# Optimization experiments

Hardware: AMD Instinct MI355X
Metric: run time of the kernel (lower is better)

## Reference

```python
import jax, jax.numpy as jnp
import numpy as np

HEADS = 16
EMBED_DIM = 1024
HEAD_DIM = EMBED_DIM // HEADS
N, Q_LEN, KV_LEN = 4, 2048, 2048


def setup_inputs() -> dict:
    key = jax.random.key(0)
    k1, k2, k3, k4, k5, k6 = jax.random.split(key, 6)
    query = jax.random.normal(k1, (N, Q_LEN, EMBED_DIM), dtype=jnp.float32)
    key_t = jax.random.normal(k2, (N, KV_LEN, EMBED_DIM), dtype=jnp.float32)
    value = jax.random.normal(k3, (N, KV_LEN, EMBED_DIM), dtype=jnp.float32)
    mask = jax.random.randint(k4, (N, 1, Q_LEN, KV_LEN), 0, 2, dtype=jnp.int32)
    # output projection (the only Linear actually used in the original forward)
    W_out = jax.random.normal(k5, (EMBED_DIM, EMBED_DIM), dtype=jnp.float32) / np.sqrt(EMBED_DIM)
    b_out = jax.random.normal(k6, (EMBED_DIM,), dtype=jnp.float32) * 0.01
    return {"query": query, "key": key_t, "value": value, "mask": mask,
            "W_out": W_out, "b_out": b_out}


def reference(query, key, value, mask, W_out, b_out):
    n, q_len, _ = query.shape
    k_len = key.shape[1]
    # split heads: [N, L, E] -> [N, L, H, D]
    q = query.reshape(n, q_len, HEADS, HEAD_DIM)
    k = key.reshape(n, k_len, HEADS, HEAD_DIM)
    v = value.reshape(n, k_len, HEADS, HEAD_DIM)
    # full QK^T scores: [N, H, Q, K]
    scores = jnp.einsum("nqhd,nkhd->nhqk", q, k)
    scores = jnp.where(mask == 0, jnp.float32(-1e9), scores)
    # non-canonical scale: 1/sqrt(embed_dim), applied AFTER masking (as original)
    attn = jax.nn.softmax(scores / jnp.sqrt(jnp.float32(EMBED_DIM)), axis=3)
    out = jnp.einsum("nhql,nlhd->nqhd", attn, v).reshape(n, q_len, HEADS * HEAD_DIM)
    return out @ W_out.T + b_out
```

## Files before the change

kernel.cpp:

```cpp
#include <hip/hip_runtime.h>
#include <stdint.h>

#define NB 4
#define QL 2048
#define KL 2048
#define HEADS 16
#define EMB 1024
#define HD 64

typedef float f32x2 __attribute__((ext_vector_type(2)));
typedef float f32x4 __attribute__((ext_vector_type(4)));
typedef float f32x16 __attribute__((ext_vector_type(16)));
typedef __bf16 bf16x2 __attribute__((ext_vector_type(2)));
typedef __bf16 bf16x8 __attribute__((ext_vector_type(8)));
typedef unsigned short u16x8 __attribute__((ext_vector_type(8)));
typedef unsigned short u16x4 __attribute__((ext_vector_type(4)));
typedef unsigned int u32x4 __attribute__((ext_vector_type(4)));

static __device__ __forceinline__ unsigned short f2bf(float f) {
  unsigned u = __float_as_uint(f);
  u += 0x7fffu + ((u >> 16) & 1u);
  return (unsigned short)(u >> 16);
}
static __device__ __forceinline__ float bf2f(unsigned short h) {
  return __uint_as_float(((unsigned)h) << 16);
}
static __device__ __forceinline__ float fast_exp2(float x) {
#if __has_builtin(__builtin_amdgcn_exp2f)
  return __builtin_amdgcn_exp2f(x);
#else
  return __expf(x * 0.6931471805599453f);
#endif
}
static __device__ __forceinline__ float fast_rcp(float x) {
#if __has_builtin(__builtin_amdgcn_rcpf)
  return __builtin_amdgcn_rcpf(x);
#else
  return 1.0f / x;
#endif
}
static __device__ __forceinline__ void dma16(const void* g, void* l) {
  __builtin_amdgcn_global_load_lds(
      (const __attribute__((address_space(1))) unsigned int*)(uintptr_t)g,
      (__attribute__((address_space(3))) unsigned int*)(uintptr_t)l, 16, 0, 0);
}
static __device__ __forceinline__ void dma4(const void* g, void* l) {
  __builtin_amdgcn_global_load_lds(
      (const __attribute__((address_space(1))) unsigned int*)(uintptr_t)g,
      (__attribute__((address_space(3))) unsigned int*)(uintptr_t)l, 4, 0, 0);
}
static __device__ __forceinline__ void barrier_plain() {
  __asm__ volatile("" ::: "memory");
  __builtin_amdgcn_s_barrier();
  __asm__ volatile("" ::: "memory");
}
#define WAITVM(N) __asm__ volatile("s_waitcnt vmcnt(" #N ")" ::: "memory")

#define XHI_OFF  0ull
#define XLO_OFF  16777216ull
#define KHI_OFF  33554432ull
#define VT_OFF   50331648ull
#define WHI_OFF  67108864ull
#define WLO_OFF  69206016ull
#define MB_OFF   71303168ull

#define QSC  0.0450842399f
#define ESHIFT 11.5415601730f

__global__ __launch_bounds__(256) void prep_all(const float* __restrict__ Kg,
                                                const float* __restrict__ Vg,
                                                const float* __restrict__ Wg,
                                                const int* __restrict__ Mg,
                                                unsigned short* __restrict__ Khi,
                                                unsigned short* __restrict__ Vt,
                                                unsigned short* __restrict__ Whi,
                                                unsigned short* __restrict__ Wlo,
                                                unsigned long long* __restrict__ bits) {
  __shared__ unsigned short lds[64 * 66];
  const int tid = threadIdx.x;
  const int bid = blockIdx.x;
  if (bid < 8192) {
    int t = bid * 256 + tid;
    int d4 = t & 15, h = (t >> 4) & 15, kv = (t >> 8) & 2047, n = t >> 19;
    f32x4 a = *(const f32x4*)(Kg + (size_t)(n * KL + kv) * EMB + h * 64 + d4 * 4);
    u16x4 o;
    #pragma unroll
    for (int j = 0; j < 4; ++j) o[j] = f2bf(a[j]);
    int row = kv & 63, c0 = d4 >> 1;
    int pos = row * 128 + ((c0 ^ (row & 7)) << 4) + (d4 & 1) * 8;
    size_t slab = (size_t)((n * 16 + h) * 32 + (kv >> 6)) * 8192;
    *(u16x4*)((char*)Khi + slab + pos) = o;
  } else if (bid < 10240) {
    int vb = bid - 8192;
    int kt = vb & 31, h = (vb >> 5) & 15, n = vb >> 9;
    #pragma unroll
    for (int i = 0; i < 4; ++i) {
      int e = i * 256 + tid;
      int d4 = e & 15, kvl = e >> 4;
      int col = (kvl & 48) | (kvl & 3) | ((kvl & 4) << 1) | ((kvl & 8) >> 1);
      f32x4 a = *(const f32x4*)(Vg + (size_t)(n * KL + kt * 64 + kvl) * EMB + h * 64 + d4 * 4);
      #pragma unroll
      for (int j = 0; j < 4; ++j) lds[(d4 * 4 + j) * 66 + col] = f2bf(a[j]);
    }
    __syncthreads();
    size_t slab = (size_t)((n * 16 + h) * 32 + kt) * 8192;
    #pragma unroll
    for (int i = 0; i < 4; ++i) {
      int e = i * 256 + tid;
      int kv4 = e & 15, d = e >> 4;
      u16x4 o;
      #pragma unroll
      for (int j = 0; j < 4; ++j) o[j] = lds[d * 66 + kv4 * 4 + j];
      int c0 = kv4 >> 1;
      int pos = d * 128 + ((c0 ^ (d & 7)) << 4) + (kv4 & 1) * 8;
      *(u16x4*)((char*)Vt + slab + pos) = o;
    }
  } else if (bid < 11264) {
    int t = (bid - 10240) * 256 + tid;
    int c4 = t & 255, row = t >> 8;
    f32x4 a = *(const f32x4*)(Wg + (size_t)row * 1024 + c4 * 4);
    u16x4 hi, lo;
    #pragma unroll
    for (int j = 0; j < 4; ++j) {
      unsigned short hb = f2bf(a[j]);
      hi[j] = hb;
      lo[j] = f2bf(a[j] - bf2f(hb));
    }
    *(u16x4*)(Whi + (size_t)row * 1024 + c4 * 4) = hi;
    *(u16x4*)(Wlo + (size_t)row * 1024 + c4 * 4) = lo;
  } else {
    int t = (bid - 11264) * 256 + tid;
    int l = t & 63;
    int W = t >> 6;
    int kw2 = (W & 15) * 2;
    int row = W >> 4;
    const int* mp = Mg + (size_t)row * KL;
    int v0 = mp[kw2 * 64 + l];
    int v1 = mp[kw2 * 64 + 64 + l];
    unsigned long long b0 = __ballot(v0 != 0);
    unsigned long long b1 = __ballot(v1 != 0);
    int q = row & 2047, nn = row >> 11;
    size_t base = (size_t)((nn * 8 + (q >> 8)) * 32) * 256 + (q & 255);
    if (l == 0) {
      bits[base + (size_t)kw2 * 256] = b0;
      bits[base + (size_t)(kw2 + 1) * 256] = b1;
    }
  }
}

__global__ __launch_bounds__(256, 2) void attn4(const float* __restrict__ Qg,
                                                const unsigned short* __restrict__ Khi,
                                                const unsigned short* __restrict__ Vt,
                                                const unsigned long long* __restrict__ Mb,
                                                unsigned short* __restrict__ Xhi,
                                                unsigned short* __restrict__ Xlo) {
  __shared__ __align__(16) char smem[2 * 18432];
  const int tid = threadIdx.x;
  const int w = tid >> 6;
  const int l = tid & 63;
  const int q32 = l & 31;
  const int h5 = l >> 5;
  const int bid = blockIdx.x;
  const int qb = bid & 7;
  const int h = (bid >> 3) & 15;
  const int n = bid >> 7;
  const int qbase = qb * 256 + w * 64;

  const char* kslab = (const char*)Khi + (size_t)(n * HEADS + h) * 262144;
  const char* vslab = (const char*)Vt + (size_t)(n * HEADS + h) * 262144;
  const char* mslab = (const char*)Mb + (size_t)(n * 8 + qb) * 65536;

  bf16x8 qh[2][4];
  #pragma unroll
  for (int c = 0; c < 2; ++c) {
    const float* qp = Qg + (size_t)(n * QL + qbase + c * 32 + q32) * EMB + h * HD + h5 * 8;
    #pragma unroll
    for (int kc = 0; kc < 4; ++kc) {
      union { u16x8 u; bf16x8 b; } H;
      #pragma unroll
      for (int j = 0; j < 8; ++j) H.u[j] = f2bf(qp[kc * 16 + j] * QSC);
      qh[c][kc] = H.b;
    }
  }
  WAITVM(0);

  int off8[2][4];
  #pragma unroll
  for (int r2 = 0; r2 < 2; ++r2)
    #pragma unroll
    for (int g = 0; g < 4; ++g)
      off8[r2][g] = (r2 * 32 + q32) * 128 + (((2 * g + h5) ^ (q32 & 7)) << 4);

  f32x16 o00, o01, o10, o11, l0, l1;
  #pragma unroll
  for (int i = 0; i < 16; ++i) {
    o00[i] = 0.f; o01[i] = 0.f; o10[i] = 0.f; o11[i] = 0.f; l0[i] = 0.f; l1[i] = 0.f;
  }

  union { u16x8 u; bf16x8 b; } O1;
  #pragma unroll
  for (int j = 0; j < 8; ++j) O1.u[j] = 0x3F80;
  const bf16x8 ones = O1.b;

  auto issue = [&](int kt, char* buf) {
    const char* ks = kslab + kt * 8192 + w * 2048 + l * 16;
    const char* vs = vslab + kt * 8192 + w * 2048 + l * 16;
    dma16(ks, buf + w * 2048);
    dma16(ks + 1024, buf + w * 2048 + 1024);
    dma16(vs, buf + 8192 + w * 2048);
    dma16(vs + 1024, buf + 8192 + w * 2048 + 1024);
    const char* ms = mslab + kt * 2048 + w * 512 + l * 4;
    dma4(ms, buf + 16384 + w * 512);
    dma4(ms + 256, buf + 16384 + w * 512 + 256);
  };

  auto step = [&](int kt, char* cur, char* nxt) {
    barrier_plain();
    if (kt != 31) {
      issue(kt + 1, nxt);
      WAITVM(6);
    } else {
      WAITVM(0);
    }
    barrier_plain();
    unsigned long long mwc0 = *(const unsigned long long*)(cur + 16384 + (w * 64 + q32) * 8);
    unsigned long long mwc1 = *(const unsigned long long*)(cur + 16384 + (w * 64 + 32 + q32) * 8);

    #pragma unroll
    for (int Mt = 0; Mt < 2; ++Mt) {
      union { u16x8 u; bf16x8 b; } kf[4];
      #pragma unroll
      for (int kc = 0; kc < 4; ++kc) kf[kc].u = *(const u16x8*)(cur + off8[Mt][kc]);

      unsigned int pk0[8], pk1[8];
      #pragma unroll
      for (int c = 0; c < 2; ++c) {
        f32x16 st;
        #pragma unroll
        for (int i = 0; i < 16; ++i) st[i] = -ESHIFT;
        #pragma unroll
        for (int kc = 0; kc < 4; ++kc)
          st = __builtin_amdgcn_mfma_f32_32x32x16_bf16(kf[kc].b, qh[c][kc], st, 0, 0, 0);
        unsigned long long mwc = c ? mwc1 : mwc0;
        unsigned int half = (unsigned int)(Mt ? (mwc >> 32) : mwc) >> (h5 * 4);
        unsigned int* pk = c ? pk1 : pk0;
        #pragma unroll
        for (int i = 0; i < 8; ++i) {
          const int r0 = 2 * i;
          const int b0 = (r0 & 3) + 8 * (r0 >> 2);
          float a0 = ((half >> b0) & 1u) ? st[r0] : -1.0e38f;
          float a1 = ((half >> (b0 + 1)) & 1u) ? st[r0 + 1] : -1.0e38f;
          float p0 = fast_exp2(a0);
          float p1 = fast_exp2(a1);
          bf16x2 pv = __builtin_convertvector((f32x2){p0, p1}, bf16x2);
          unsigned int u;
          __builtin_memcpy(&u, &pv, 4);
          pk[i] = u;
        }
      }
      #pragma unroll
      for (int kc2 = 0; kc2 < 2; ++kc2) {
        const int kvc = Mt * 2 + kc2;
        union { u16x8 u; bf16x8 b; } vf0, vf1;
        vf0.u = *(const u16x8*)(cur + 8192 + off8[0][kvc]);
        vf1.u = *(const u16x8*)(cur + 8192 + off8[1][kvc]);
        union { u32x4 wv; bf16x8 b; } pf0, pf1;
        #pragma unroll
        for (int j = 0; j < 4; ++j) {
          pf0.wv[j] = pk0[4 * kc2 + j];
          pf1.wv[j] = pk1[4 * kc2 + j];
        }
        o00 = __builtin_amdgcn_mfma_f32_32x32x16_bf16(pf0.b, vf0.b, o00, 0, 0, 0);
        o01 = __builtin_amdgcn_mfma_f32_32x32x16_bf16(pf0.b, vf1.b, o01, 0, 0, 0);
        l0  = __builtin_amdgcn_mfma_f32_32x32x16_bf16(pf0.b, ones,  l0,  0, 0, 0);
        o10 = __builtin_amdgcn_mfma_f32_32x32x16_bf16(pf1.b, vf0.b, o10, 0, 0, 0);
        o11 = __builtin_amdgcn_mfma_f32_32x32x16_bf16(pf1.b, vf1.b, o11, 0, 0, 0);
        l1  = __builtin_amdgcn_mfma_f32_32x32x16_bf16(pf1.b, ones,  l1,  0, 0, 0);
      }
    }
  };

  issue(0, smem);
  for (int kt2 = 0; kt2 < 16; ++kt2) {
    step(2 * kt2, smem, smem + 18432);
    step(2 * kt2 + 1, smem + 18432, smem);
  }

  #pragma unroll
  for (int c = 0; c < 2; ++c) {
    const f32x16& oa = c ? o10 : o00;
    const f32x16& ob = c ? o11 : o01;
    const f32x16& ll = c ? l1 : l0;
    #pragma unroll
    for (int r = 0; r < 16; ++r) {
      float inv = fast_rcp(ll[r]);
      int qr = (r & 3) + 8 * (r >> 2) + 4 * h5;
      size_t base = (size_t)(n * QL + qbase + c * 32 + qr) * EMB + h * HD + q32;
      float v0 = oa[r] * inv;
      unsigned short h0 = f2bf(v0);
      Xhi[base] = h0;
      Xlo[base] = f2bf(v0 - bf2f(h0));
      float v1 = ob[r] * inv;
      unsigned short h1 = f2bf(v1);
      Xhi[base + 32] = h1;
      Xlo[base + 32] = f2bf(v1 - bf2f(h1));
    }
  }
}

__global__ __launch_bounds__(256, 2) void proj3(const unsigned short* __restrict__ Xhi,
                                                const unsigned short* __restrict__ Xlo,
                                                const unsigned short* __restrict__ Whi,
                                                const unsigned short* __restrict__ Wlo,
                                                const float* __restrict__ bias,
                                                float* __restrict__ out) {
  __shared__ __align__(16) char pm[65536];
  const int tid = threadIdx.x;
  const int w = tid >> 6;
  const int l = tid & 63;
  const int lr = l & 15;
  const int lq = l >> 4;
  const int wm = w >> 1, wn = w & 1;
  const int bid = blockIdx.x;
  const int m0 = (bid >> 3) * 128;
  const int n0 = (bid & 7) * 128;

  f32x4 acc[4][4];
  #pragma unroll
  for (int i = 0; i < 4; ++i)
    #pragma unroll
    for (int j = 0; j < 4; ++j) acc[i][j] = (f32x4){0.f, 0.f, 0.f, 0.f};

  auto issue = [&](int kc, char* buf) {
    #pragma unroll
    for (int i = 0; i < 8; ++i) {
      int s = (i * 256 + tid) * 16;
      int sel = s >> 13;
      int s2 = s & 8191;
      int row = s2 >> 6;
      int c = (s2 >> 4) & 3;
      const unsigned short* pl = sel == 0 ? Xhi : sel == 1 ? Xlo : sel == 2 ? Whi : Wlo;
      int rbase = (sel < 2 ? m0 : n0) + row;
      dma16(pl + (size_t)rbase * 1024 + kc * 32 + c * 8, buf + i * 4096 + w * 1024);
    }
  };

  auto pstep = [&](int kc, char* cur, char* nxt) {
    barrier_plain();
    if (kc != 31) {
      issue(kc + 1, nxt);
      WAITVM(8);
    } else {
      WAITVM(0);
    }
    barrier_plain();

    bf16x8 ah[4], al[4], bh[4], bl[4];
    #pragma unroll
    for (int mt = 0; mt < 4; ++mt) {
      int off = (wm * 64 + mt * 16 + lr) * 64 + lq * 16;
      union { u16x8 u; bf16x8 b; } A, B;
      A.u = *(const u16x8*)(cur + off);
      B.u = *(const u16x8*)(cur + 8192 + off);
      ah[mt] = A.b;
      al[mt] = B.b;
    }
    #pragma unroll
    for (int nt = 0; nt < 4; ++nt) {
      int off = (wn * 64 + nt * 16 + lr) * 64 + lq * 16;
      union { u16x8 u; bf16x8 b; } A, B;
      A.u = *(const u16x8*)(cur + 16384 + off);
      B.u = *(const u16x8*)(cur + 24576 + off);
      bh[nt] = A.b;
      bl[nt] = B.b;
    }
    #pragma unroll
    for (int mt = 0; mt < 4; ++mt)
      #pragma unroll
      for (int nt = 0; nt < 4; ++nt) {
        f32x4 c = acc[mt][nt];
        c = __builtin_amdgcn_mfma_f32_16x16x32_bf16(ah[mt], bh[nt], c, 0, 0, 0);
        c = __builtin_amdgcn_mfma_f32_16x16x32_bf16(ah[mt], bl[nt], c, 0, 0, 0);
        c = __builtin_amdgcn_mfma_f32_16x16x32_bf16(al[mt], bh[nt], c, 0, 0, 0);
        acc[mt][nt] = c;
      }
  };

  issue(0, pm);
  for (int kc2 = 0; kc2 < 16; ++kc2) {
    pstep(2 * kc2, pm, pm + 32768);
    pstep(2 * kc2 + 1, pm + 32768, pm);
  }

  #pragma unroll
  for (int nt = 0; nt < 4; ++nt) {
    int col = n0 + wn * 64 + nt * 16 + lr;
    float bv = bias[col];
    #pragma unroll
    for (int mt = 0; mt < 4; ++mt) {
      int rowb = m0 + wm * 64 + mt * 16 + lq * 4;
      #pragma unroll
      for (int r = 0; r < 4; ++r)
        out[(size_t)(rowb + r) * EMB + col] = acc[mt][nt][r] + bv;
    }
  }
}

extern "C" void kernel_launch(void* const* d_in, const int* in_sizes, int n_in,
                              void* d_out, int out_size, void* d_ws, size_t ws_size,
                              hipStream_t stream) {
  const float* Qg = (const float*)d_in[0];
  const float* Kg = (const float*)d_in[1];
  const float* Vg = (const float*)d_in[2];
  const int* Mg = (const int*)d_in[3];
  const float* Wg = (const float*)d_in[4];
  const float* Bg = (const float*)d_in[5];
  float* out = (float*)d_out;

  char* ws = (char*)d_ws;
  unsigned short* xhi = (unsigned short*)(ws + XHI_OFF);
  unsigned short* xlo = (unsigned short*)(ws + XLO_OFF);
  unsigned short* khi = (unsigned short*)(ws + KHI_OFF);
  unsigned short* vt = (unsigned short*)(ws + VT_OFF);
  unsigned short* whi = (unsigned short*)(ws + WHI_OFF);
  unsigned short* wlo = (unsigned short*)(ws + WLO_OFF);
  unsigned long long* mbits = (unsigned long long*)(ws + MB_OFF);

  prep_all<<<44032, 256, 0, stream>>>(Kg, Vg, Wg, Mg, khi, vt, whi, wlo, mbits);
  attn4<<<NB * HEADS * (QL / 256), 256, 0, stream>>>(Qg, khi, vt, mbits, xhi, xlo);
  proj3<<<(NB * QL / 128) * (EMB / 128), 256, 0, stream>>>(xhi, xlo, whi, wlo, Bg, out);
}
```

Before: 320.2 us.

## Halve attention query tile per wave to raise occupancy, add MFMA priority hints

Each wave now handles 32 query rows instead of 64, which halves the accumulator registers, and the block covers 128 queries. That allows launch bounds of 4 blocks per SM and doubles the grid. Block IDs are remapped so consecutive blocks spread across heads and batches, and s_setprio is raised around the MFMA groups. The cost is that each K/V tile loaded into shared memory is reused by half as many query rows, so K/V traffic from L2 doubles.

```diff
diff --git a/kernel.cpp b/kernel.cpp
--- a/kernel.cpp
+++ b/kernel.cpp
@@ -148,38 +148,39 @@
   }
 }
 
-__global__ __launch_bounds__(256, 2) void attn4(const float* __restrict__ Qg,
+__global__ __launch_bounds__(256, 4) void attn4(const float* __restrict__ Qg,
                                                 const unsigned short* __restrict__ Khi,
                                                 const unsigned short* __restrict__ Vt,
                                                 const unsigned long long* __restrict__ Mb,
                                                 unsigned short* __restrict__ Xhi,
                                                 unsigned short* __restrict__ Xlo) {
-  __shared__ __align__(16) char smem[2 * 18432];
+  __shared__ __align__(16) char smem[2 * 17408];
   const int tid = threadIdx.x;
   const int w = tid >> 6;
   const int l = tid & 63;
   const int q32 = l & 31;
   const int h5 = l >> 5;
-  const int bid = blockIdx.x;
-  const int qb = bid & 7;
-  const int h = (bid >> 3) & 15;
-  const int n = bid >> 7;
-  const int qbase = qb * 256 + w * 64;
+  const int bid0 = blockIdx.x;
+  const int bid = (bid0 & 7) * 128 + (bid0 >> 3);
+  const int qb = bid & 15;
+  const int h = (bid >> 4) & 15;
+  const int n = bid >> 8;
+  const int qbase = qb * 128 + w * 32;
 
   const char* kslab = (const char*)Khi + (size_t)(n * HEADS + h) * 262144;
   const char* vslab = (const char*)Vt + (size_t)(n * HEADS + h) * 262144;
-  const char* mslab = (const char*)Mb + (size_t)(n * 8 + qb) * 65536;
-
-  bf16x8 qh[2][4];
-  #pragma unroll
-  for (int c = 0; c < 2; ++c) {
-    const float* qp = Qg + (size_t)(n * QL + qbase + c * 32 + q32) * EMB + h * HD + h5 * 8;
+  const char* mslab = (const char*)Mb + (size_t)(n * 8 + (qb >> 1)) * 65536 +
+                      (size_t)(qb & 1) * 1024;
+
+  bf16x8 qh[4];
+  {
+    const float* qp = Qg + (size_t)(n * QL + qbase + q32) * EMB + h * HD + h5 * 8;
     #pragma unroll
     for (int kc = 0; kc < 4; ++kc) {
       union { u16x8 u; bf16x8 b; } H;
       #pragma unroll
       for (int j = 0; j < 8; ++j) H.u[j] = f2bf(qp[kc * 16 + j] * QSC);
-      qh[c][kc] = H.b;
+      qh[kc] = H.b;
     }
   }
   WAITVM(0);
@@ -191,11 +192,9 @@
     for (int g = 0; g < 4; ++g)
       off8[r2][g] = (r2 * 32 + q32) * 128 + (((2 * g + h5) ^ (q32 & 7)) << 4);
 
-  f32x16 o00, o01, o10, o11, l0, l1;
-  #pragma unroll
-  for (int i = 0; i < 16; ++i) {
-    o00[i] = 0.f; o01[i] = 0.f; o10[i] = 0.f; o11[i] = 0.f; l0[i] = 0.f; l1[i] = 0.f;
-  }
+  f32x16 o0, o1, la;
+  #pragma unroll
+  for (int i = 0; i < 16; ++i) { o0[i] = 0.f; o1[i] = 0.f; la[i] = 0.f; }
 
   union { u16x8 u; bf16x8 b; } O1;
   #pragma unroll
@@ -209,22 +208,19 @@
     dma16(ks + 1024, buf + w * 2048 + 1024);
     dma16(vs, buf + 8192 + w * 2048);
     dma16(vs + 1024, buf + 8192 + w * 2048 + 1024);
-    const char* ms = mslab + kt * 2048 + w * 512 + l * 4;
-    dma4(ms, buf + 16384 + w * 512);
-    dma4(ms + 256, buf + 16384 + w * 512 + 256);
+    dma4(mslab + kt * 2048 + w * 256 + l * 4, buf + 16384 + w * 256);
   };
 
   auto step = [&](int kt, char* cur, char* nxt) {
     barrier_plain();
     if (kt != 31) {
       issue(kt + 1, nxt);
-      WAITVM(6);
+      WAITVM(5);
     } else {
       WAITVM(0);
     }
     barrier_plain();
-    unsigned long long mwc0 = *(const unsigned long long*)(cur + 16384 + (w * 64 + q32) * 8);
-    unsigned long long mwc1 = *(const unsigned long long*)(cur + 16384 + (w * 64 + 32 + q32) * 8);
+    unsigned long long mw = *(const unsigned long long*)(cur + 16384 + (w * 32 + q32) * 8);
 
     #pragma unroll
     for (int Mt = 0; Mt < 2; ++Mt) {
@@ -232,31 +228,29 @@
       #pragma unroll
       for (int kc = 0; kc < 4; ++kc) kf[kc].u = *(const u16x8*)(cur + off8[Mt][kc]);
 
-      unsigned int pk0[8], pk1[8];
-      #pragma unroll
-      for (int c = 0; c < 2; ++c) {
-        f32x16 st;
-        #pragma unroll
-        for (int i = 0; i < 16; ++i) st[i] = -ESHIFT;
-        #pragma unroll
-        for (int kc = 0; kc < 4; ++kc)
-          st = __builtin_amdgcn_mfma_f32_32x32x16_bf16(kf[kc].b, qh[c][kc], st, 0, 0, 0);
-        unsigned long long mwc = c ? mwc1 : mwc0;
-        unsigned int half = (unsigned int)(Mt ? (mwc >> 32) : mwc) >> (h5 * 4);
-        unsigned int* pk = c ? pk1 : pk0;
-        #pragma unroll
-        for (int i = 0; i < 8; ++i) {
-          const int r0 = 2 * i;
-          const int b0 = (r0 & 3) + 8 * (r0 >> 2);
-          float a0 = ((half >> b0) & 1u) ? st[r0] : -1.0e38f;
-          float a1 = ((half >> (b0 + 1)) & 1u) ? st[r0 + 1] : -1.0e38f;
-          float p0 = fast_exp2(a0);
-          float p1 = fast_exp2(a1);
-          bf16x2 pv = __builtin_convertvector((f32x2){p0, p1}, bf16x2);
-          unsigned int u;
-          __builtin_memcpy(&u, &pv, 4);
-          pk[i] = u;
-        }
+      f32x16 st;
+      #pragma unroll
+      for (int i = 0; i < 16; ++i) st[i] = -ESHIFT;
+      __builtin_amdgcn_s_setprio(1);
+      #pragma unroll
+      for (int kc = 0; kc < 4; ++kc)
+        st = __builtin_amdgcn_mfma_f32_32x32x16_bf16(kf[kc].b, qh[kc], st, 0, 0, 0);
+      __builtin_amdgcn_s_setprio(0);
+
+      unsigned int half = (unsigned int)(Mt ? (mw >> 32) : mw) >> (h5 * 4);
+      unsigned int pk[8];
+      #pragma unroll
+      for (int i = 0; i < 8; ++i) {
+        const int r0 = 2 * i;
+        const int b0 = (r0 & 3) + 8 * (r0 >> 2);
+        float a0 = ((half >> b0) & 1u) ? st[r0] : -1.0e38f;
+        float a1 = ((half >> (b0 + 1)) & 1u) ? st[r0 + 1] : -1.0e38f;
+        float p0 = fast_exp2(a0);
+        float p1 = fast_exp2(a1);
+        bf16x2 pv = __builtin_convertvector((f32x2){p0, p1}, bf16x2);
+        unsigned int u;
+        __builtin_memcpy(&u, &pv, 4);
+        pk[i] = u;
       }
       #pragma unroll
       for (int kc2 = 0; kc2 < 2; ++kc2) {
@@ -264,47 +258,37 @@
         union { u16x8 u; bf16x8 b; } vf0, vf1;
         vf0.u = *(const u16x8*)(cur + 8192 + off8[0][kvc]);
         vf1.u = *(const u16x8*)(cur + 8192 + off8[1][kvc]);
-        union { u32x4 wv; bf16x8 b; } pf0, pf1;
+        union { u32x4 wv; bf16x8 b; } pf;
         #pragma unroll
-        for (int j = 0; j < 4; ++j) {
-          pf0.wv[j] = pk0[4 * kc2 + j];
-          pf1.wv[j] = pk1[4 * kc2 + j];
-        }
-        o00 = __builtin_amdgcn_mfma_f32_32x32x16_bf16(pf0.b, vf0.b, o00, 0, 0, 0);
-        o01 = __builtin_amdgcn_mfma_f32_32x32x16_bf16(pf0.b, vf1.b, o01, 0, 0, 0);
-        l0  = __builtin_amdgcn_mfma_f32_32x32x16_bf16(pf0.b, ones,  l0,  0, 0, 0);
-        o10 = __builtin_amdgcn_mfma_f32_32x32x16_bf16(pf1.b, vf0.b, o10, 0, 0, 0);
-        o11 = __builtin_amdgcn_mfma_f32_32x32x16_bf16(pf1.b, vf1.b, o11, 0, 0, 0);
-        l1  = __builtin_amdgcn_mfma_f32_32x32x16_bf16(pf1.b, ones,  l1,  0, 0, 0);
+        for (int j = 0; j < 4; ++j) pf.wv[j] = pk[4 * kc2 + j];
+        __builtin_amdgcn_s_setprio(1);
+        o0 = __builtin_amdgcn_mfma_f32_32x32x16_bf16(pf.b, vf0.b, o0, 0, 0, 0);
+        o1 = __builtin_amdgcn_mfma_f32_32x32x16_bf16(pf.b, vf1.b, o1, 0, 0, 0);
+        la = __builtin_amdgcn_mfma_f32_32x32x16_bf16(pf.b, ones, la, 0, 0, 0);
+        __builtin_amdgcn_s_setprio(0);
       }
     }
   };
 
   issue(0, smem);
   for (int kt2 = 0; kt2 < 16; ++kt2) {
-    step(2 * kt2, smem, smem + 18432);
-    step(2 * kt2 + 1, smem + 18432, smem);
-  }
-
-  #pragma unroll
-  for (int c = 0; c < 2; ++c) {
-    const f32x16& oa = c ? o10 : o00;
-    const f32x16& ob = c ? o11 : o01;
-    const f32x16& ll = c ? l1 : l0;
-    #pragma unroll
-    for (int r = 0; r < 16; ++r) {
-      float inv = fast_rcp(ll[r]);
-      int qr = (r & 3) + 8 * (r >> 2) + 4 * h5;
-      size_t base = (size_t)(n * QL + qbase + c * 32 + qr) * EMB + h * HD + q32;
-      float v0 = oa[r] * inv;
-      unsigned short h0 = f2bf(v0);
-      Xhi[base] = h0;
-      Xlo[base] = f2bf(v0 - bf2f(h0));
-      float v1 = ob[r] * inv;
-      unsigned short h1 = f2bf(v1);
-      Xhi[base + 32] = h1;
-      Xlo[base + 32] = f2bf(v1 - bf2f(h1));
-    }
+    step(2 * kt2, smem, smem + 17408);
+    step(2 * kt2 + 1, smem + 17408, smem);
+  }
+
+  #pragma unroll
+  for (int r = 0; r < 16; ++r) {
+    float inv = fast_rcp(la[r]);
+    int qr = (r & 3) + 8 * (r >> 2) + 4 * h5;
+    size_t base = (size_t)(n * QL + qbase + qr) * EMB + h * HD + q32;
+    float v0 = o0[r] * inv;
+    unsigned short h0 = f2bf(v0);
+    Xhi[base] = h0;
+    Xlo[base] = f2bf(v0 - bf2f(h0));
+    float v1 = o1[r] * inv;
+    unsigned short h1 = f2bf(v1);
+    Xhi[base + 32] = h1;
+    Xlo[base + 32] = f2bf(v1 - bf2f(h1));
   }
 }
 
@@ -427,6 +411,6 @@
   unsigned long long* mbits = (unsigned long long*)(ws + MB_OFF);
 
   prep_all<<<44032, 256, 0, stream>>>(Kg, Vg, Wg, Mg, khi, vt, whi, wlo, mbits);
-  attn4<<<NB * HEADS * (QL / 256), 256, 0, stream>>>(Qg, khi, vt, mbits, xhi, xlo);
+  attn4<<<NB * HEADS * (QL / 128), 256, 0, stream>>>(Qg, khi, vt, mbits, xhi, xlo);
   proj3<<<(NB * QL / 128) * (EMB / 128), 256, 0, stream>>>(xhi, xlo, whi, wlo, Bg, out);
 }
```

Measured after the change: 362.7 us. +13.3%, slower.
